# Performance work log

Hardware: AMD Instinct MI355X
Metric: run time of the kernel (lower is better)

Reference implementation:

```python
import jax, jax.numpy as jnp
import numpy as np

B, Q, S, T, HID, NH = 4, 64, 64, 128, 768, 12
HD = HID // NH  # 64
SCALE = 1.0 / (HD ** 0.5)
EPS = 1e-12


def setup_inputs() -> dict:
    key = jax.random.key(0)
    ks = jax.random.split(key, 12)
    std = 0.02
    return {
        "ini_q": jax.random.normal(ks[0], (B, Q, HID), jnp.float32),
        "ini_k": jax.random.normal(ks[1], (B, S, T, HID), jnp.float32),
        "mask": jax.random.randint(ks[2], (B, S, T), 0, 2).astype(jnp.float32),
        "Wq": jax.random.normal(ks[3], (HID, HID), jnp.float32) * std,
        "bq": jnp.zeros((HID,), jnp.float32),
        "Wk": jax.random.normal(ks[4], (HID, HID), jnp.float32) * std,
        "bk": jnp.zeros((HID,), jnp.float32),
        "Wv": jax.random.normal(ks[5], (HID, HID), jnp.float32) * std,
        "bv": jnp.zeros((HID,), jnp.float32),
        "Wo": jax.random.normal(ks[6], (HID, HID), jnp.float32) * std,
        "bo": jnp.zeros((HID,), jnp.float32),
        "gamma": jnp.ones((HID,), jnp.float32),
        "beta": jnp.zeros((HID,), jnp.float32),
    }


def reference(ini_q, ini_k, mask, Wq, bq, Wk, bk, Wv, bv, Wo, bo, gamma, beta):
    b, q_num, _ = ini_q.shape
    _, s_num, t_num, _ = ini_k.shape
    # projections (torch Linear: x @ W.T + b; here W stored pre-transposed)
    q = (ini_q @ Wq + bq).reshape(b, q_num, NH, HD)          # [b,q,h,d]
    k = (ini_k @ Wk + bk).reshape(b, s_num, t_num, NH, HD)   # [b,s,t,h,d]
    v = (ini_k @ Wv + bv).reshape(b, s_num, t_num, NH, HD)
    # non-aligned path: scores [b,h,q,s,t]
    scores = jnp.einsum('bqhd,bsthd->bhqst', q, k) * SCALE
    scores = scores + mask[:, None, None, :, :] * (-10000.0)
    alpha = jax.nn.softmax(scores, axis=-1)
    res = jnp.einsum('bhqst,bsthd->bqshd', alpha, v)          # [b,q,s,h,d]
    res = res.reshape(b, q_num, s_num, NH * HD)
    res = res @ Wo + bo                                        # [b,q,s,hid]
    # LayerNorm over last dim
    mu = jnp.mean(res, axis=-1, keepdims=True)
    var = jnp.var(res, axis=-1, keepdims=True)
    return (res - mu) / jnp.sqrt(var + EPS) * gamma + beta
```

## Files before the change

### kernel.cpp

```cpp
#include <hip/hip_runtime.h>
#include <cstdint>
#include <cstddef>
#include <type_traits>

#define HID 768
#define NB 4
#define NQ 64
#define NS 64
#define NT 128
#define NHEAD 12
#define HD 64

typedef __attribute__((ext_vector_type(8))) short bf16x8;
typedef __attribute__((ext_vector_type(4))) float f32x4;

__device__ __forceinline__ unsigned short f2bf(float f) {
    union { float f; uint32_t u; } c; c.f = f;
    uint32_t x = c.u;
    uint32_t r = (x + 0x7FFFu + ((x >> 16) & 1u)) >> 16;
    return (unsigned short)r;
}

__device__ __forceinline__ f32x4 mfma16(bf16x8 a, bf16x8 b, f32x4 c) {
    return __builtin_amdgcn_mfma_f32_16x16x32_bf16(a, b, c, 0, 0, 0);
}

__device__ __forceinline__ void gload_lds16(const void* g, void* l) {
    __builtin_amdgcn_global_load_lds(
        (const __attribute__((address_space(1))) unsigned int*)g,
        (__attribute__((address_space(3))) unsigned int*)l, 16, 0, 0);
}

__global__ __launch_bounds__(256) void cast4_f32_bf16(const float* __restrict__ in,
                                                      unsigned short* __restrict__ out, int n4) {
    int i = blockIdx.x * 256 + threadIdx.x;
    if (i < n4) {
        float4 v = ((const float4*)in)[i];
        ushort4 o;
        o.x = f2bf(v.x); o.y = f2bf(v.y); o.z = f2bf(v.z); o.w = f2bf(v.w);
        ((ushort4*)out)[i] = o;
    }
}

__global__ __launch_bounds__(256) void transpose_cast_768(const float* __restrict__ W,
                                                          unsigned short* __restrict__ Wt) {
    __shared__ float t[32][33];
    int bx = blockIdx.x % 24, by = blockIdx.x / 24;
    int n0 = bx * 32, k0 = by * 32;
    int tx = threadIdx.x & 31, ty = threadIdx.x >> 5;
#pragma unroll
    for (int i = 0; i < 4; ++i)
        t[ty + i * 8][tx] = W[(size_t)(k0 + ty + i * 8) * 768 + n0 + tx];
    __syncthreads();
#pragma unroll
    for (int i = 0; i < 4; ++i)
        Wt[(size_t)(n0 + ty + i * 8) * 768 + k0 + tx] = f2bf(t[tx][ty + i * 8]);
}

template <typename CT, bool SPLIT>
__global__ __launch_bounds__(256) void gemm_bt_2ph(const unsigned short* __restrict__ A,
                                                   const unsigned short* __restrict__ Bt,
                                                   const float* __restrict__ bias0,
                                                   const float* __restrict__ bias1,
                                                   CT* __restrict__ C0,
                                                   CT* __restrict__ C1,
                                                   int ncb) {
    constexpr int K = 768;
    constexpr int NKT = K / 32;
    __shared__ __align__(16) unsigned short As[2][128 * 32];
    __shared__ __align__(16) unsigned short Bs[2][128 * 32];

    int tid = threadIdx.x;
    int w = tid >> 6, l = tid & 63;
    int li = l & 15, g = l >> 4;
    int wm = w >> 1, wn = w & 1;

    int nwg = gridDim.x, bid = blockIdx.x;
    if ((nwg & 7) == 0) {
        int cpx = nwg >> 3;
        bid = (bid & 7) * cpx + (bid >> 3);
    }
    int nb = bid % ncb, mb = bid / ncb;

    const unsigned short* Ab = A + (size_t)mb * 128 * K;
    const unsigned short* Bb = Bt + (size_t)nb * 128 * K;

    int ch0 = w * 128 + l, ch1 = ch0 + 64;
    int r0 = ch0 >> 2, c0 = ch0 & 3;
    int r1 = ch1 >> 2, c1 = ch1 & 3;

#define STAGE(bufi, kt)                                                              \
    do {                                                                             \
        int k0_ = (kt) * 32;                                                         \
        gload_lds16(Ab + (size_t)r0 * K + k0_ + c0 * 8,                              \
                    (char*)(&As[bufi][0]) + w * 2048);                               \
        gload_lds16(Ab + (size_t)r1 * K + k0_ + c1 * 8,                              \
                    (char*)(&As[bufi][0]) + w * 2048 + 1024);                        \
        gload_lds16(Bb + (size_t)r0 * K + k0_ + c0 * 8,                              \
                    (char*)(&Bs[bufi][0]) + w * 2048);                               \
        gload_lds16(Bb + (size_t)r1 * K + k0_ + c1 * 8,                              \
                    (char*)(&Bs[bufi][0]) + w * 2048 + 1024);                        \
    } while (0)

    f32x4 acc[4][4];
#pragma unroll
    for (int mi = 0; mi < 4; ++mi)
#pragma unroll
        for (int ni = 0; ni < 4; ++ni) acc[mi][ni] = (f32x4){0.f, 0.f, 0.f, 0.f};

#define COMPUTE(bufi)                                                                \
    do {                                                                             \
        bf16x8 af[4], bb[4];                                                         \
        _Pragma("unroll") for (int mi = 0; mi < 4; ++mi)                             \
            af[mi] = *(const bf16x8*)&As[bufi][(wm * 64 + mi * 16 + li) * 32 + g * 8];\
        _Pragma("unroll") for (int ni = 0; ni < 4; ++ni)                             \
            bb[ni] = *(const bf16x8*)&Bs[bufi][(wn * 64 + ni * 16 + li) * 32 + g * 8];\
        _Pragma("unroll") for (int mi = 0; mi < 4; ++mi)                             \
            _Pragma("unroll") for (int ni = 0; ni < 4; ++ni)                         \
                acc[mi][ni] = mfma16(af[mi], bb[ni], acc[mi][ni]);                   \
    } while (0)

    STAGE(0, 0);
    __syncthreads();
    for (int kt = 0; kt < NKT - 2; kt += 2) {
        STAGE(1, kt + 1);
        COMPUTE(0);
        __syncthreads();
        STAGE(0, kt + 2);
        COMPUTE(1);
        __syncthreads();
    }
    STAGE(1, NKT - 1);
    COMPUTE(0);
    __syncthreads();
    COMPUTE(1);
#undef STAGE
#undef COMPUTE

    int rowb = mb * 128 + wm * 64;
    int colb = nb * 128 + wn * 64;
#pragma unroll
    for (int ni = 0; ni < 4; ++ni) {
        int col = colb + ni * 16 + li;
        CT* Cp;
        float bv;
        int ccol;
        if (SPLIT && col >= 768) {
            Cp = C1; bv = bias1[col - 768]; ccol = col - 768;
        } else {
            Cp = C0; bv = bias0[col]; ccol = col;
        }
#pragma unroll
        for (int mi = 0; mi < 4; ++mi) {
#pragma unroll
            for (int r = 0; r < 4; ++r) {
                int row = rowb + mi * 16 + g * 4 + r;
                float v = acc[mi][ni][r] + bv;
                if constexpr (std::is_same_v<CT, unsigned short>)
                    Cp[(size_t)row * 768 + ccol] = f2bf(v);
                else
                    Cp[(size_t)row * 768 + ccol] = v;
            }
        }
    }
}

__global__ __launch_bounds__(256) void attn_bsh(const unsigned short* __restrict__ Qp,
                                                const unsigned short* __restrict__ Kb,
                                                const unsigned short* __restrict__ Vb,
                                                const float* __restrict__ mask,
                                                unsigned short* __restrict__ res) {
    __shared__ __align__(16) unsigned short Kl[128 * 72];
    __shared__ __align__(16) unsigned short VT[64 * 136];
    __shared__ __align__(16) unsigned short QA[64 * 136];

    int bid = blockIdx.x;
    int h = bid % NHEAD;
    int bs = bid / NHEAD;
    int s = bs % NS;
    int b = bs / NS;

    int tid = threadIdx.x, w = tid >> 6, l = tid & 63;
    int li = l & 15, g = l >> 4;

    const unsigned short* Qg = Qp + (size_t)(b * NQ) * HID + h * HD;
#pragma unroll
    for (int it = 0; it < 2; ++it) {
        int idx = it * 256 + tid;
        int q = idx >> 3, c = idx & 7;
        *(uint4*)&QA[q * 72 + c * 8] = *(const uint4*)&Qg[(size_t)q * HID + c * 8];
    }
    const unsigned short* Kg = Kb + ((size_t)(b * NS + s) * NT) * HID + h * HD;
#pragma unroll
    for (int it = 0; it < 4; ++it) {
        int idx = it * 256 + tid;
        int t = idx >> 3, c = idx & 7;
        *(uint4*)&Kl[t * 72 + c * 8] = *(const uint4*)&Kg[(size_t)t * HID + c * 8];
    }
    const unsigned short* Vg = Vb + ((size_t)(b * NS + s) * NT) * HID + h * HD;
#pragma unroll
    for (int it = 0; it < 4; ++it) {
        int idx = it * 256 + tid;
        int t = idx >> 3, c = idx & 7;
        uint4 raw = *(const uint4*)&Vg[(size_t)t * HID + c * 8];
        const unsigned short* e = (const unsigned short*)&raw;
#pragma unroll
        for (int j = 0; j < 8; ++j) VT[(c * 8 + j) * 136 + t] = e[j];
    }
    __syncthreads();

    bf16x8 aq0 = *(const bf16x8*)&QA[(w * 16 + li) * 72 + g * 8];
    bf16x8 aq1 = *(const bf16x8*)&QA[(w * 16 + li) * 72 + 32 + g * 8];
    f32x4 sc[8];
#pragma unroll
    for (int tc = 0; tc < 8; ++tc) {
        sc[tc] = (f32x4){0.f, 0.f, 0.f, 0.f};
        bf16x8 b0 = *(const bf16x8*)&Kl[(tc * 16 + li) * 72 + g * 8];
        sc[tc] = mfma16(aq0, b0, sc[tc]);
        bf16x8 b1 = *(const bf16x8*)&Kl[(tc * 16 + li) * 72 + 32 + g * 8];
        sc[tc] = mfma16(aq1, b1, sc[tc]);
    }

    const float* mrow = mask + (size_t)(b * NS + s) * NT;
    float mv[8];
#pragma unroll
    for (int tc = 0; tc < 8; ++tc) mv[tc] = mrow[tc * 16 + li] * -10000.0f;

    float p[8][4];
    float rmax[4] = {-3.0e38f, -3.0e38f, -3.0e38f, -3.0e38f};
#pragma unroll
    for (int tc = 0; tc < 8; ++tc)
#pragma unroll
        for (int r = 0; r < 4; ++r) {
            float v = sc[tc][r] * 0.125f + mv[tc];
            p[tc][r] = v;
            rmax[r] = fmaxf(rmax[r], v);
        }
#pragma unroll
    for (int r = 0; r < 4; ++r)
#pragma unroll
        for (int m = 1; m < 16; m <<= 1)
            rmax[r] = fmaxf(rmax[r], __shfl_xor(rmax[r], m, 64));

    float rsum[4] = {0.f, 0.f, 0.f, 0.f};
#pragma unroll
    for (int tc = 0; tc < 8; ++tc)
#pragma unroll
        for (int r = 0; r < 4; ++r) {
            float e = __expf(p[tc][r] - rmax[r]);
            p[tc][r] = e;
            rsum[r] += e;
        }
#pragma unroll
    for (int r = 0; r < 4; ++r)
#pragma unroll
        for (int m = 1; m < 16; m <<= 1)
            rsum[r] += __shfl_xor(rsum[r], m, 64);
    float rinv[4];
#pragma unroll
    for (int r = 0; r < 4; ++r) rinv[r] = 1.0f / rsum[r];

    __syncthreads();
#pragma unroll
    for (int tc = 0; tc < 8; ++tc)
#pragma unroll
        for (int r = 0; r < 4; ++r)
            QA[(w * 16 + g * 4 + r) * 136 + tc * 16 + li] = f2bf(p[tc][r] * rinv[r]);
    __syncthreads();

    bf16x8 pa[4];
#pragma unroll
    for (int ks = 0; ks < 4; ++ks)
        pa[ks] = *(const bf16x8*)&QA[(w * 16 + li) * 136 + ks * 32 + g * 8];
    f32x4 o[4];
#pragma unroll
    for (int dc = 0; dc < 4; ++dc) {
        o[dc] = (f32x4){0.f, 0.f, 0.f, 0.f};
#pragma unroll
        for (int ks = 0; ks < 4; ++ks) {
            bf16x8 bv = *(const bf16x8*)&VT[(dc * 16 + li) * 136 + ks * 32 + g * 8];
            o[dc] = mfma16(pa[ks], bv, o[dc]);
        }
    }

#pragma unroll
    for (int dc = 0; dc < 4; ++dc) {
#pragma unroll
        for (int r = 0; r < 4; ++r) {
            int q = w * 16 + g * 4 + r;
            int d = dc * 16 + li;
            res[((size_t)(b * NQ + q) * NS + s) * HID + h * HD + d] = f2bf(o[dc][r]);
        }
    }
}

__global__ __launch_bounds__(256) void ln_768(const float* __restrict__ X,
                                              const float* __restrict__ gamma,
                                              const float* __restrict__ beta,
                                              float* __restrict__ out) {
    int w = threadIdx.x >> 6, l = threadIdx.x & 63;
    size_t row = (size_t)blockIdx.x * 4 + w;
    const float4* xr = (const float4*)(X + row * 768);
    float4 v[3];
    float s = 0.f, sq = 0.f;
#pragma unroll
    for (int j = 0; j < 3; ++j) {
        v[j] = xr[l + j * 64];
        s += v[j].x + v[j].y + v[j].z + v[j].w;
        sq += v[j].x * v[j].x + v[j].y * v[j].y + v[j].z * v[j].z + v[j].w * v[j].w;
    }
#pragma unroll
    for (int m = 32; m >= 1; m >>= 1) {
        s += __shfl_xor(s, m, 64);
        sq += __shfl_xor(sq, m, 64);
    }
    float mu = s * (1.0f / 768.0f);
    float var = sq * (1.0f / 768.0f) - mu * mu;
    float rstd = rsqrtf(fmaxf(var, 0.0f) + 1e-12f);
    const float4* g4 = (const float4*)gamma;
    const float4* b4 = (const float4*)beta;
    float4* o4 = (float4*)(out + row * 768);
#pragma unroll
    for (int j = 0; j < 3; ++j) {
        float4 gg = g4[l + j * 64], bb = b4[l + j * 64];
        float4 r;
        r.x = (v[j].x - mu) * rstd * gg.x + bb.x;
        r.y = (v[j].y - mu) * rstd * gg.y + bb.y;
        r.z = (v[j].z - mu) * rstd * gg.z + bb.z;
        r.w = (v[j].w - mu) * rstd * gg.w + bb.w;
        o4[l + j * 64] = r;
    }
}

extern "C" void kernel_launch(void* const* d_in, const int* in_sizes, int n_in,
                              void* d_out, int out_size, void* d_ws, size_t ws_size,
                              hipStream_t stream) {
    const float* ini_q = (const float*)d_in[0];
    const float* ini_k = (const float*)d_in[1];
    const float* mask  = (const float*)d_in[2];
    const float* Wq = (const float*)d_in[3];
    const float* bq = (const float*)d_in[4];
    const float* Wk = (const float*)d_in[5];
    const float* bk = (const float*)d_in[6];
    const float* Wv = (const float*)d_in[7];
    const float* bv = (const float*)d_in[8];
    const float* Wo = (const float*)d_in[9];
    const float* bo = (const float*)d_in[10];
    const float* gamma = (const float*)d_in[11];
    const float* beta  = (const float*)d_in[12];
    float* out = (float*)d_out;

    constexpr size_t SZ_X = (size_t)32768 * 768 * 2;
    constexpr size_t SZ_R = (size_t)16384 * 768 * 2;
    constexpr size_t SZ_Q = (size_t)256 * 768 * 2;
    constexpr size_t SZ_W = (size_t)768 * 768 * 2;

    char* base = (char*)d_ws;
    unsigned short* X   = (unsigned short*)(base);
    unsigned short* Kb  = (unsigned short*)(base + SZ_X);
    unsigned short* Vb  = (unsigned short*)(base + 2 * SZ_X);
    unsigned short* res = (unsigned short*)(base + 3 * SZ_X);
    unsigned short* Xq  = (unsigned short*)(base + 3 * SZ_X + SZ_R);
    unsigned short* Qp  = (unsigned short*)(base + 3 * SZ_X + SZ_R + SZ_Q);
    unsigned short* WqT = (unsigned short*)(base + 3 * SZ_X + SZ_R + 2 * SZ_Q);
    unsigned short* KVt = (unsigned short*)((char*)WqT + SZ_W);
    unsigned short* WoT = (unsigned short*)((char*)WqT + 3 * SZ_W);
    float* res2 = (float*)(base);

    cast4_f32_bf16<<<24576, 256, 0, stream>>>(ini_k, X, 6291456);
    cast4_f32_bf16<<<192, 256, 0, stream>>>(ini_q, Xq, 49152);
    transpose_cast_768<<<576, 256, 0, stream>>>(Wq, WqT);
    transpose_cast_768<<<576, 256, 0, stream>>>(Wk, KVt);
    transpose_cast_768<<<576, 256, 0, stream>>>(Wv, KVt + 768 * 768);
    transpose_cast_768<<<576, 256, 0, stream>>>(Wo, WoT);

    gemm_bt_2ph<unsigned short, false><<<dim3(2 * 6), 256, 0, stream>>>(
        Xq, WqT, bq, nullptr, Qp, nullptr, 6);
    gemm_bt_2ph<unsigned short, true><<<dim3(256 * 12), 256, 0, stream>>>(
        X, KVt, bk, bv, Kb, Vb, 12);

    attn_bsh<<<dim3(NB * NS * NHEAD), 256, 0, stream>>>(Qp, Kb, Vb, mask, res);

    gemm_bt_2ph<float, false><<<dim3(128 * 6), 256, 0, stream>>>(
        res, WoT, bo, nullptr, res2, nullptr, 6);
    ln_768<<<dim3(4096), 256, 0, stream>>>(res2, gamma, beta, out);
}
```

Baseline: 425.1 us.

## Fuse fp32-to-bf16 cast into GEMM A loads, use 256-row tiles, batch weight transposes

Drops the standalone cast kernels for ini_k and ini_q. The GEMM now loads fp32 activations into registers, packs them to bf16 and writes them to LDS itself, which avoids writing and re-reading a large bf16 copy of the K/V input. The GEMM tile grows to 256x128 with 512 threads, and the four weight transpose-cast launches are merged into one. The register-staged A path is software pipelined across the compute step, but it adds VALU conversion work and register pressure under the new launch bounds.

```diff
diff --git a/kernel.cpp b/kernel.cpp
--- a/kernel.cpp
+++ b/kernel.cpp
@@ -1,4 +1,5 @@
 #include <hip/hip_runtime.h>
+#include <hip/hip_bf16.h>
 #include <cstdint>
 #include <cstddef>
 #include <type_traits>
@@ -31,21 +32,25 @@
         (__attribute__((address_space(3))) unsigned int*)l, 16, 0, 0);
 }
 
-__global__ __launch_bounds__(256) void cast4_f32_bf16(const float* __restrict__ in,
-                                                      unsigned short* __restrict__ out, int n4) {
-    int i = blockIdx.x * 256 + threadIdx.x;
-    if (i < n4) {
-        float4 v = ((const float4*)in)[i];
-        ushort4 o;
-        o.x = f2bf(v.x); o.y = f2bf(v.y); o.z = f2bf(v.z); o.w = f2bf(v.w);
-        ((ushort4*)out)[i] = o;
-    }
-}
-
-__global__ __launch_bounds__(256) void transpose_cast_768(const float* __restrict__ W,
-                                                          unsigned short* __restrict__ Wt) {
+__device__ __forceinline__ bf16x8 pack8(float4 x, float4 y) {
+    bf16x8 r;
+    r[0] = (short)f2bf(x.x); r[1] = (short)f2bf(x.y);
+    r[2] = (short)f2bf(x.z); r[3] = (short)f2bf(x.w);
+    r[4] = (short)f2bf(y.x); r[5] = (short)f2bf(y.y);
+    r[6] = (short)f2bf(y.z); r[7] = (short)f2bf(y.w);
+    return r;
+}
+
+__global__ __launch_bounds__(256) void transpose_cast_4x768(
+    const float* __restrict__ W0, const float* __restrict__ W1,
+    const float* __restrict__ W2, const float* __restrict__ W3,
+    unsigned short* __restrict__ D0, unsigned short* __restrict__ D1,
+    unsigned short* __restrict__ D2, unsigned short* __restrict__ D3) {
     __shared__ float t[32][33];
-    int bx = blockIdx.x % 24, by = blockIdx.x / 24;
+    int wi = blockIdx.x / 576, bb = blockIdx.x % 576;
+    const float* W = (wi == 0) ? W0 : (wi == 1) ? W1 : (wi == 2) ? W2 : W3;
+    unsigned short* D = (wi == 0) ? D0 : (wi == 1) ? D1 : (wi == 2) ? D2 : D3;
+    int bx = bb % 24, by = bb / 24;
     int n0 = bx * 32, k0 = by * 32;
     int tx = threadIdx.x & 31, ty = threadIdx.x >> 5;
 #pragma unroll
@@ -54,20 +59,20 @@
     __syncthreads();
 #pragma unroll
     for (int i = 0; i < 4; ++i)
-        Wt[(size_t)(n0 + ty + i * 8) * 768 + k0 + tx] = f2bf(t[tx][ty + i * 8]);
-}
-
-template <typename CT, bool SPLIT>
-__global__ __launch_bounds__(256) void gemm_bt_2ph(const unsigned short* __restrict__ A,
-                                                   const unsigned short* __restrict__ Bt,
-                                                   const float* __restrict__ bias0,
-                                                   const float* __restrict__ bias1,
-                                                   CT* __restrict__ C0,
-                                                   CT* __restrict__ C1,
-                                                   int ncb) {
+        D[(size_t)(n0 + ty + i * 8) * 768 + k0 + tx] = f2bf(t[tx][ty + i * 8]);
+}
+
+template <typename AT, typename CT, bool SPLIT>
+__global__ __launch_bounds__(512, 4) void gemm256_2ph(const AT* __restrict__ A,
+                                                      const unsigned short* __restrict__ Bt,
+                                                      const float* __restrict__ bias0,
+                                                      const float* __restrict__ bias1,
+                                                      CT* __restrict__ C0,
+                                                      CT* __restrict__ C1,
+                                                      int ncb) {
     constexpr int K = 768;
     constexpr int NKT = K / 32;
-    __shared__ __align__(16) unsigned short As[2][128 * 32];
+    __shared__ __align__(16) unsigned short As[2][256 * 32];
     __shared__ __align__(16) unsigned short Bs[2][128 * 32];
 
     int tid = threadIdx.x;
@@ -82,24 +87,45 @@
     }
     int nb = bid % ncb, mb = bid / ncb;
 
-    const unsigned short* Ab = A + (size_t)mb * 128 * K;
+    const AT* Ab = A + (size_t)mb * 256 * K;
     const unsigned short* Bb = Bt + (size_t)nb * 128 * K;
 
-    int ch0 = w * 128 + l, ch1 = ch0 + 64;
-    int r0 = ch0 >> 2, c0 = ch0 & 3;
-    int r1 = ch1 >> 2, c1 = ch1 & 3;
-
-#define STAGE(bufi, kt)                                                              \
+    int br = tid >> 2, bc = tid & 3;
+    int ar = tid >> 1, ah = tid & 1;
+
+    float4 a4[4];
+
+#define STAGE_B(bufi, kt)                                                            \
+    gload_lds16(Bb + (size_t)br * K + (kt) * 32 + bc * 8,                            \
+                (char*)(&Bs[bufi][0]) + w * 1024)
+
+#define STAGE_A16(bufi, kt)                                                          \
     do {                                                                             \
-        int k0_ = (kt) * 32;                                                         \
-        gload_lds16(Ab + (size_t)r0 * K + k0_ + c0 * 8,                              \
-                    (char*)(&As[bufi][0]) + w * 2048);                               \
-        gload_lds16(Ab + (size_t)r1 * K + k0_ + c1 * 8,                              \
-                    (char*)(&As[bufi][0]) + w * 2048 + 1024);                        \
-        gload_lds16(Bb + (size_t)r0 * K + k0_ + c0 * 8,                              \
-                    (char*)(&Bs[bufi][0]) + w * 2048);                               \
-        gload_lds16(Bb + (size_t)r1 * K + k0_ + c1 * 8,                              \
-                    (char*)(&Bs[bufi][0]) + w * 2048 + 1024);                        \
+        gload_lds16(Ab + (size_t)(tid >> 2) * K + (kt) * 32 + (tid & 3) * 8,         \
+                    (char*)(&As[bufi][0]) + w * 1024);                               \
+        gload_lds16(Ab + (size_t)(128 + (tid >> 2)) * K + (kt) * 32 + (tid & 3) * 8, \
+                    (char*)(&As[bufi][0]) + 8192 + w * 1024);                        \
+    } while (0)
+
+#define GLOADA(kt)                                                                   \
+    do {                                                                             \
+        const float4* s_ = (const float4*)(Ab + (size_t)ar * K + (kt) * 32 + ah * 16);\
+        a4[0] = s_[0]; a4[1] = s_[1]; a4[2] = s_[2]; a4[3] = s_[3];                  \
+    } while (0)
+
+#define STAGE_ALL(bufi, kt)                                                          \
+    do {                                                                             \
+        if constexpr (std::is_same_v<AT, float>) GLOADA(kt);                         \
+        else STAGE_A16(bufi, kt);                                                    \
+        STAGE_B(bufi, kt);                                                           \
+    } while (0)
+
+#define FINISH_A(bufi)                                                               \
+    do {                                                                             \
+        if constexpr (std::is_same_v<AT, float>) {                                   \
+            *(bf16x8*)&As[bufi][ar * 32 + ah * 16] = pack8(a4[0], a4[1]);            \
+            *(bf16x8*)&As[bufi][ar * 32 + ah * 16 + 8] = pack8(a4[2], a4[3]);        \
+        }                                                                            \
     } while (0)
 
     f32x4 acc[4][4];
@@ -120,24 +146,32 @@
                 acc[mi][ni] = mfma16(af[mi], bb[ni], acc[mi][ni]);                   \
     } while (0)
 
-    STAGE(0, 0);
+    STAGE_ALL(0, 0);
+    FINISH_A(0);
     __syncthreads();
     for (int kt = 0; kt < NKT - 2; kt += 2) {
-        STAGE(1, kt + 1);
+        STAGE_ALL(1, kt + 1);
         COMPUTE(0);
+        FINISH_A(1);
         __syncthreads();
-        STAGE(0, kt + 2);
+        STAGE_ALL(0, kt + 2);
         COMPUTE(1);
+        FINISH_A(0);
         __syncthreads();
     }
-    STAGE(1, NKT - 1);
+    STAGE_ALL(1, NKT - 1);
     COMPUTE(0);
+    FINISH_A(1);
     __syncthreads();
     COMPUTE(1);
-#undef STAGE
+#undef STAGE_B
+#undef STAGE_A16
+#undef GLOADA
+#undef STAGE_ALL
+#undef FINISH_A
 #undef COMPUTE
 
-    int rowb = mb * 128 + wm * 64;
+    int rowb = mb * 256 + wm * 64;
     int colb = nb * 128 + wn * 64;
 #pragma unroll
     for (int ni = 0; ni < 4; ++ni) {
@@ -350,38 +384,32 @@
     const float* beta  = (const float*)d_in[12];
     float* out = (float*)d_out;
 
-    constexpr size_t SZ_X = (size_t)32768 * 768 * 2;
-    constexpr size_t SZ_R = (size_t)16384 * 768 * 2;
-    constexpr size_t SZ_Q = (size_t)256 * 768 * 2;
-    constexpr size_t SZ_W = (size_t)768 * 768 * 2;
+    constexpr size_t SZ_KV = (size_t)32768 * 768 * 2;
+    constexpr size_t SZ_R  = (size_t)16384 * 768 * 2;
+    constexpr size_t SZ_Q  = (size_t)256 * 768 * 2;
+    constexpr size_t SZ_W  = (size_t)768 * 768 * 2;
 
     char* base = (char*)d_ws;
-    unsigned short* X   = (unsigned short*)(base);
-    unsigned short* Kb  = (unsigned short*)(base + SZ_X);
-    unsigned short* Vb  = (unsigned short*)(base + 2 * SZ_X);
-    unsigned short* res = (unsigned short*)(base + 3 * SZ_X);
-    unsigned short* Xq  = (unsigned short*)(base + 3 * SZ_X + SZ_R);
-    unsigned short* Qp  = (unsigned short*)(base + 3 * SZ_X + SZ_R + SZ_Q);
-    unsigned short* WqT = (unsigned short*)(base + 3 * SZ_X + SZ_R + 2 * SZ_Q);
+    unsigned short* Kb  = (unsigned short*)(base);
+    unsigned short* Vb  = (unsigned short*)(base + SZ_KV);
+    unsigned short* res = (unsigned short*)(base + 2 * SZ_KV);
+    unsigned short* Qp  = (unsigned short*)(base + 2 * SZ_KV + SZ_R);
+    unsigned short* WqT = (unsigned short*)(base + 2 * SZ_KV + SZ_R + SZ_Q);
     unsigned short* KVt = (unsigned short*)((char*)WqT + SZ_W);
     unsigned short* WoT = (unsigned short*)((char*)WqT + 3 * SZ_W);
     float* res2 = (float*)(base);
 
-    cast4_f32_bf16<<<24576, 256, 0, stream>>>(ini_k, X, 6291456);
-    cast4_f32_bf16<<<192, 256, 0, stream>>>(ini_q, Xq, 49152);
-    transpose_cast_768<<<576, 256, 0, stream>>>(Wq, WqT);
-    transpose_cast_768<<<576, 256, 0, stream>>>(Wk, KVt);
-    transpose_cast_768<<<576, 256, 0, stream>>>(Wv, KVt + 768 * 768);
-    transpose_cast_768<<<576, 256, 0, stream>>>(Wo, WoT);
-
-    gemm_bt_2ph<unsigned short, false><<<dim3(2 * 6), 256, 0, stream>>>(
-        Xq, WqT, bq, nullptr, Qp, nullptr, 6);
-    gemm_bt_2ph<unsigned short, true><<<dim3(256 * 12), 256, 0, stream>>>(
-        X, KVt, bk, bv, Kb, Vb, 12);
+    transpose_cast_4x768<<<4 * 576, 256, 0, stream>>>(
+        Wq, Wk, Wv, Wo, WqT, KVt, KVt + 768 * 768, WoT);
+
+    gemm256_2ph<float, unsigned short, false><<<6, 512, 0, stream>>>(
+        ini_q, WqT, bq, nullptr, Qp, nullptr, 6);
+    gemm256_2ph<float, unsigned short, true><<<128 * 12, 512, 0, stream>>>(
+        ini_k, KVt, bk, bv, Kb, Vb, 12);
 
     attn_bsh<<<dim3(NB * NS * NHEAD), 256, 0, stream>>>(Qp, Kb, Vb, mask, res);
 
-    gemm_bt_2ph<float, false><<<dim3(128 * 6), 256, 0, stream>>>(
+    gemm256_2ph<unsigned short, float, false><<<64 * 6, 512, 0, stream>>>(
         res, WoT, bo, nullptr, res2, nullptr, 6);
     ln_768<<<dim3(4096), 256, 0, stream>>>(res2, gamma, beta, out);
 }
```

After: 452.1 us. +6.3%, slower.
